# Kernel tuning notes

Measured on AMD Instinct MI355X. Metric: run time of the kernel, lower is better.

The kernel has to match this reference:

```python
import jax, jax.numpy as jnp
import numpy as np

K_DIM = 1024
HEADS = 16
D_K = K_DIM // HEADS


def setup_inputs() -> dict:
    key = jax.random.key(0)
    ks = jax.random.split(key, 6)
    b, t, k = 4, 1024, K_DIM
    scale = 1.0 / np.sqrt(k)
    return {
        "x": jax.random.normal(ks[0], (b, t, k), dtype=jnp.float32),
        "Wq": jax.random.normal(ks[1], (k, k), dtype=jnp.float32) * scale,
        "Wk": jax.random.normal(ks[2], (k, k), dtype=jnp.float32) * scale,
        "Wv": jax.random.normal(ks[3], (k, k), dtype=jnp.float32) * scale,
        "Wo": jax.random.normal(ks[4], (k, k), dtype=jnp.float32) * scale,
        "bo": jax.random.normal(ks[5], (k,), dtype=jnp.float32) * 0.01,
    }


def reference(x, Wq, Wk, Wv, Wo, bo):
    b, t, k = x.shape
    h, d_k = HEADS, D_K
    # Linear(k,k) applies x @ W.T; project then split heads -> [b, h, t, d_k]
    Q = (x @ Wq.T).reshape(b, t, h, d_k).transpose(0, 2, 1, 3)
    Kh = (x @ Wk.T).reshape(b, t, h, d_k).transpose(0, 2, 1, 3)
    V = (x @ Wv.T).reshape(b, t, h, d_k).transpose(0, 2, 1, 3)
    scores = jnp.einsum("bhqd,bhkd->bhqk", Q, Kh) / jnp.sqrt(jnp.float32(d_k))
    attn = jax.nn.softmax(scores, axis=-1)
    out = jnp.einsum("bhqk,bhkd->bhqd", attn, V)
    out = out.transpose(0, 2, 1, 3).reshape(b, t, k)
    return out @ Wo.T + bo
```

## Files before the change

kernel.cpp:

```cpp
#include <hip/hip_runtime.h>
#include <hip/hip_bf16.h>

typedef __attribute__((ext_vector_type(4))) float f32x4;
typedef __attribute__((ext_vector_type(8))) short short8;

#define B_   4
#define T_   1024
#define H_   16
#define DK_  64
#define KDIM 1024

#define QSCALE 0.18033688011112042f

__device__ __forceinline__ unsigned short f2bf(float f){
  union { float f; unsigned int u; } a; a.f = f;
  unsigned int u = a.u;
  return (unsigned short)((u + 0x7FFFu + ((u >> 16) & 1u)) >> 16);
}

__device__ __forceinline__ unsigned int cvtpk_bf16(float lo, float hi){
  unsigned int r;
  asm("v_cvt_pk_bf16_f32 %0, %1, %2" : "=v"(r) : "v"(lo), "v"(hi));
  return r;
}

__device__ __forceinline__ void gload16(const void* g, void* l){
  __builtin_amdgcn_global_load_lds(
      (const __attribute__((address_space(1))) unsigned int*)g,
      (__attribute__((address_space(3))) unsigned int*)l,
      16, 0, 0);
}

__global__ __launch_bounds__(256) void convert5(
    const float* __restrict__ x,  const float* __restrict__ wq,
    const float* __restrict__ wk, const float* __restrict__ wv,
    const float* __restrict__ wo,
    short* __restrict__ xb,  short* __restrict__ wqb,
    short* __restrict__ wkb, short* __restrict__ wvb, short* __restrict__ wob)
{
  int i = blockIdx.x * 256 + threadIdx.x;
  const float* s; short* d; int off;
  if (i < (1 << 20)) { s = x; d = xb; off = i; }
  else {
    int j = i - (1 << 20);
    int w = j >> 18;
    off = j & ((1 << 18) - 1);
    s = (w == 0) ? wq : (w == 1) ? wk : (w == 2) ? wv : wo;
    d = (w == 0) ? wqb : (w == 1) ? wkb : (w == 2) ? wvb : wob;
  }
  float4 v = ((const float4*)s)[off];
  ushort4 o;
  o.x = f2bf(v.x); o.y = f2bf(v.y); o.z = f2bf(v.z); o.w = f2bf(v.w);
  ((ushort4*)d)[off] = o;
}

template<bool SWAP>
__device__ __forceinline__ void gemm3_core(
    const short* __restrict__ A, const short* __restrict__ W,
    int m0, int n0, short* As, short* Bs, f32x4 acc[4][2])
{
  const int tid = threadIdx.x, wv = tid >> 6, lane = tid & 63;
  const int lr = lane & 15, lq = lane >> 4;
  const int wm = wv >> 2, wn = wv & 3;
  const int swz = (lr & 7) << 3;
  const int r = tid >> 3;
  const int c8 = ((tid & 7) * 8) ^ ((r & 7) * 8);

#pragma unroll
  for (int m = 0; m < 4; ++m)
#pragma unroll
    for (int n = 0; n < 2; ++n) acc[m][n] = (f32x4){0.f, 0.f, 0.f, 0.f};

  auto stage = [&](int sb, int kt) {
    const int k0 = kt * 64;
#pragma unroll
    for (int p = 0; p < 2; ++p) {
      const int rp = p * 64 + r;
      gload16(A + (size_t)(m0 + rp) * KDIM + k0 + c8, As + sb * 8192 + p * 4096 + wv * 512);
      gload16(W + (size_t)(n0 + rp) * KDIM + k0 + c8, Bs + sb * 8192 + p * 4096 + wv * 512);
    }
  };

  stage(0, 0);
  stage(1, 1);

  for (int kt = 0; kt < 16; ++kt) {
    if (kt < 15) asm volatile("s_waitcnt vmcnt(4)" ::: "memory");
    else         asm volatile("s_waitcnt vmcnt(0)" ::: "memory");
    __builtin_amdgcn_s_barrier();
    __builtin_amdgcn_sched_barrier(0);
    const int rb = kt % 3;
    const short* Ab = As + rb * 8192;
    const short* Bb = Bs + rb * 8192;
    short8 af[2][4], bfv[2][2];
#pragma unroll
    for (int kk = 0; kk < 2; ++kk) {
#pragma unroll
      for (int m = 0; m < 4; ++m)
        af[kk][m] = *(const short8*)(Ab + (wm * 64 + m * 16 + lr) * 64 + ((kk * 32 + lq * 8) ^ swz));
#pragma unroll
      for (int n = 0; n < 2; ++n)
        bfv[kk][n] = *(const short8*)(Bb + (wn * 32 + n * 16 + lr) * 64 + ((kk * 32 + lq * 8) ^ swz));
    }
    if (kt + 2 < 16) {
      const int sb = (kt + 2) % 3;
      stage(sb, kt + 2);
    }
    __builtin_amdgcn_s_setprio(1);
#pragma unroll
    for (int kk = 0; kk < 2; ++kk)
#pragma unroll
      for (int m = 0; m < 4; ++m)
#pragma unroll
        for (int n = 0; n < 2; ++n) {
          if constexpr (SWAP)
            acc[m][n] = __builtin_amdgcn_mfma_f32_16x16x32_bf16(bfv[kk][n], af[kk][m], acc[m][n], 0, 0, 0);
          else
            acc[m][n] = __builtin_amdgcn_mfma_f32_16x16x32_bf16(af[kk][m], bfv[kk][n], acc[m][n], 0, 0, 0);
        }
    __builtin_amdgcn_s_setprio(0);
  }
}

__global__ __launch_bounds__(512, 1) void gemm3_qkv(
    const short* __restrict__ xb,
    const short* __restrict__ Wqb, const short* __restrict__ Wkb, const short* __restrict__ Wvb,
    short* __restrict__ Qb, short* __restrict__ Kb, short* __restrict__ VTb)
{
  __shared__ __align__(16) short As[3 * 8192];
  __shared__ __align__(16) short Bs[3 * 8192];
  const int bid = blockIdx.x;
  const int wgid = (bid & 7) * 96 + (bid >> 3);
  const int mx = wgid / 24, inner = wgid % 24;
  const int wsel = inner >> 3;
  const int m0 = mx * 128, n0 = (inner & 7) * 128;
  const short* W = (wsel == 0) ? Wqb : (wsel == 1) ? Wkb : Wvb;

  const int tid = threadIdx.x, lane = tid & 63, wv = tid >> 6;
  const int lr = lane & 15, lq = lane >> 4;
  const int wm = wv >> 2, wn = wv & 3;

  if (wsel < 2) {
    f32x4 acc[4][2];
    gemm3_core<true>(xb, W, m0, n0, As, Bs, acc);
    short* O = wsel ? Kb : Qb;
    const float sc = wsel ? 1.0f : QSCALE;
#pragma unroll
    for (int m = 0; m < 4; ++m) {
      const int row = m0 + wm * 64 + m * 16 + lr;
#pragma unroll
      for (int n = 0; n < 2; ++n) {
        const int colb = n0 + wn * 32 + n * 16 + lq * 4;
        ushort4 u;
        u.x = f2bf(acc[m][n][0] * sc); u.y = f2bf(acc[m][n][1] * sc);
        u.z = f2bf(acc[m][n][2] * sc); u.w = f2bf(acc[m][n][3] * sc);
        *(ushort4*)&O[(size_t)row * KDIM + colb] = u;
      }
    }
  } else {
    f32x4 acc[4][2];
    gemm3_core<false>(xb, W, m0, n0, As, Bs, acc);
#pragma unroll
    for (int m = 0; m < 4; ++m)
#pragma unroll
      for (int n = 0; n < 2; ++n) {
        int row = m0 + wm * 64 + m * 16 + lq * 4;
        int col = n0 + wn * 32 + n * 16 + lr;
        int b = row >> 10, t = row & 1023, h = col >> 6, d = col & 63;
        int tp = (t & ~31) + ((t >> 2) & 3) * 8 + ((t >> 4) & 1) * 4 + (t & 3);
        ushort4 v;
        v.x = f2bf(acc[m][n][0]); v.y = f2bf(acc[m][n][1]);
        v.z = f2bf(acc[m][n][2]); v.w = f2bf(acc[m][n][3]);
        *(ushort4*)&VTb[(size_t)((b * 16 + h) * 64 + d) * 1024 + tp] = v;
      }
  }
}

__global__ __launch_bounds__(512, 1) void gemm3_out(
    const short* __restrict__ AOb, const short* __restrict__ Wob,
    const float* __restrict__ bias, float* __restrict__ out)
{
  __shared__ __align__(16) short As[3 * 8192];
  __shared__ __align__(16) short Bs[3 * 8192];
  const int bid = blockIdx.x;
  const int wgid = (bid & 7) * 32 + (bid >> 3);
  const int mx = wgid >> 3, ny = wgid & 7;
  const int m0 = mx * 128, n0 = ny * 128;

  f32x4 acc[4][2];
  gemm3_core<true>(AOb, Wob, m0, n0, As, Bs, acc);

  const int tid = threadIdx.x, lane = tid & 63, wv = tid >> 6;
  const int lr = lane & 15, lq = lane >> 4;
  const int wm = wv >> 2, wn = wv & 3;
#pragma unroll
  for (int n = 0; n < 2; ++n) {
    const int colb = n0 + wn * 32 + n * 16 + lq * 4;
    const float4 bv = *(const float4*)&bias[colb];
#pragma unroll
    for (int m = 0; m < 4; ++m) {
      const int row = m0 + wm * 64 + m * 16 + lr;
      float4 o;
      o.x = acc[m][n][0] + bv.x; o.y = acc[m][n][1] + bv.y;
      o.z = acc[m][n][2] + bv.z; o.w = acc[m][n][3] + bv.w;
      *(float4*)&out[(size_t)row * KDIM + colb] = o;
    }
  }
}

__global__ __launch_bounds__(256) void attn_kern(
    const short* __restrict__ Qb, const short* __restrict__ Kb,
    const short* __restrict__ VTb, short* __restrict__ AOb)
{
  __shared__ __align__(16) short kl[2][64 * 64];
  __shared__ __align__(16) short vl[2][64 * 64];
  const int flat = blockIdx.x;
  const int wg = (flat & 7) * 128 + (flat >> 3);
  const int bh = wg >> 4, b = bh >> 4, h = bh & 15;
  const int q0 = (wg & 15) * 64;
  const int tid = threadIdx.x, wv = tid >> 6, lane = tid & 63;
  const int lr = lane & 15, lq = lane >> 4;

  const short* Qrow = Qb + (size_t)(b * T_ + q0 + wv * 16 + lr) * KDIM + h * DK_;
  short8 qf0 = *(const short8*)(Qrow + lq * 8);
  short8 qf1 = *(const short8*)(Qrow + 32 + lq * 8);

  const short* Kbase = Kb + (size_t)(b * T_) * KDIM + h * DK_;
  const short* Vbase = VTb + (size_t)(bh * DK_) * 1024;

  const int srow = tid >> 3, scol = (tid & 7) * 8;

  auto stage = [&](int buf, int kv0) {
#pragma unroll
    for (int p = 0; p < 2; ++p) {
      const int r = p * 32 + srow;
      gload16(Kbase + (size_t)(kv0 + r) * KDIM + (scol ^ ((r & 7) << 3)),
              &kl[buf][p * 2048 + wv * 512]);
    }
#pragma unroll
    for (int p = 0; p < 2; ++p) {
      const int r = p * 32 + srow;
      gload16(Vbase + (size_t)r * 1024 + kv0 + (scol ^ ((r & 7) << 3)),
              &vl[buf][p * 2048 + wv * 512]);
    }
  };

  f32x4 oacc[4];
#pragma unroll
  for (int i = 0; i < 4; ++i) oacc[i] = (f32x4){0.f, 0.f, 0.f, 0.f};
  float l_r = 0.f;

  int cur = 0;
  stage(0, 0);
  __syncthreads();

  for (int kt = 0; kt < 16; ++kt) {
    if (kt < 15) stage(cur ^ 1, (kt + 1) * 64);

    f32x4 s[4];
#pragma unroll
    for (int nt = 0; nt < 4; ++nt) {
      const int kr = nt * 16 + lr;
      const int swr = (kr & 7) << 3;
      short8 kf0 = *(const short8*)&kl[cur][kr * 64 + ((lq * 8) ^ swr)];
      short8 kf1 = *(const short8*)&kl[cur][kr * 64 + ((32 + lq * 8) ^ swr)];
      f32x4 z = (f32x4){0.f, 0.f, 0.f, 0.f};
      z = __builtin_amdgcn_mfma_f32_16x16x32_bf16(kf0, qf0, z, 0, 0, 0);
      s[nt] = __builtin_amdgcn_mfma_f32_16x16x32_bf16(kf1, qf1, z, 0, 0, 0);
    }

    float rs = 0.f;
#pragma unroll
    for (int nt = 0; nt < 4; ++nt)
#pragma unroll
      for (int j = 0; j < 4; ++j) {
        float e = exp2f(s[nt][j]);
        s[nt][j] = e;
        rs += e;
      }
    l_r += rs;

    union { unsigned int u[4]; short8 v; } pk0, pk1;
    pk0.u[0] = cvtpk_bf16(s[0][0], s[0][1]);
    pk0.u[1] = cvtpk_bf16(s[0][2], s[0][3]);
    pk0.u[2] = cvtpk_bf16(s[1][0], s[1][1]);
    pk0.u[3] = cvtpk_bf16(s[1][2], s[1][3]);
    pk1.u[0] = cvtpk_bf16(s[2][0], s[2][1]);
    pk1.u[1] = cvtpk_bf16(s[2][2], s[2][3]);
    pk1.u[2] = cvtpk_bf16(s[3][0], s[3][1]);
    pk1.u[3] = cvtpk_bf16(s[3][2], s[3][3]);

#pragma unroll
    for (int ntd = 0; ntd < 4; ++ntd) {
      const int vr = ntd * 16 + lr;
      const int swr = (vr & 7) << 3;
      short8 vf0 = *(const short8*)&vl[cur][vr * 64 + ((lq * 8) ^ swr)];
      short8 vf1 = *(const short8*)&vl[cur][vr * 64 + ((32 + lq * 8) ^ swr)];
      oacc[ntd] = __builtin_amdgcn_mfma_f32_16x16x32_bf16(vf0, pk0.v, oacc[ntd], 0, 0, 0);
      oacc[ntd] = __builtin_amdgcn_mfma_f32_16x16x32_bf16(vf1, pk1.v, oacc[ntd], 0, 0, 0);
    }
    __syncthreads();
    cur ^= 1;
  }

  float l = l_r;
  l += __shfl_xor(l, 16);
  l += __shfl_xor(l, 32);
  const float inv = 1.0f / l;

#pragma unroll
  for (int nt = 0; nt < 4; ++nt) {
    ushort4 u;
    u.x = f2bf(oacc[nt][0] * inv);
    u.y = f2bf(oacc[nt][1] * inv);
    u.z = f2bf(oacc[nt][2] * inv);
    u.w = f2bf(oacc[nt][3] * inv);
    *(ushort4*)&AOb[(size_t)(b * T_ + q0 + wv * 16 + lr) * KDIM + h * DK_ + nt * 16 + lq * 4] = u;
  }
}

extern "C" void kernel_launch(void* const* d_in, const int* in_sizes, int n_in,
                              void* d_out, int out_size, void* d_ws, size_t ws_size,
                              hipStream_t stream) {
  const float* x  = (const float*)d_in[0];
  const float* Wq = (const float*)d_in[1];
  const float* Wk = (const float*)d_in[2];
  const float* Wv = (const float*)d_in[3];
  const float* Wo = (const float*)d_in[4];
  const float* bo = (const float*)d_in[5];

  short* ws = (short*)d_ws;
  short* xb  = ws;
  short* Wqb = ws + 4194304;
  short* Wkb = ws + 5242880;
  short* Wvb = ws + 6291456;
  short* Wob = ws + 7340032;
  short* Qb  = ws + 8388608;
  short* Kb  = ws + 12582912;
  short* VTb = ws + 16777216;
  short* AOb = ws + 20971520;

  convert5<<<8192, 256, 0, stream>>>(x, Wq, Wk, Wv, Wo, xb, Wqb, Wkb, Wvb, Wob);
  gemm3_qkv<<<768, 512, 0, stream>>>(xb, Wqb, Wkb, Wvb, Qb, Kb, VTb);
  attn_kern<<<1024, 256, 0, stream>>>(Qb, Kb, VTb, AOb);
  gemm3_out<<<256, 512, 0, stream>>>(AOb, Wob, bo, (float*)d_out);
}
```

Measured before the change: 168.6 us.

## Process two query tiles per warp in attention and fold Q scale into weights

Each attention warp now handles 32 query rows as two 16-row groups instead of 16, so each K/V fragment read from LDS feeds twice as many MFMAs. The grid is halved to 512 blocks of 128 queries, which cuts redundant K/V staging but raises register pressure and lowers the number of blocks. The softmax scale for Q now multiplies Wq during the bf16 conversion rather than the QKV GEMM epilogue. That moves the multiply to a cheaper place and slightly changes rounding.

Result: no change. 168.0 us (-0.4%).

```diff
diff --git a/kernel.cpp b/kernel.cpp
--- a/kernel.cpp
+++ b/kernel.cpp
@@ -40,6 +40,7 @@
 {
   int i = blockIdx.x * 256 + threadIdx.x;
   const float* s; short* d; int off;
+  float sc = 1.0f;
   if (i < (1 << 20)) { s = x; d = xb; off = i; }
   else {
     int j = i - (1 << 20);
@@ -47,10 +48,12 @@
     off = j & ((1 << 18) - 1);
     s = (w == 0) ? wq : (w == 1) ? wk : (w == 2) ? wv : wo;
     d = (w == 0) ? wqb : (w == 1) ? wkb : (w == 2) ? wvb : wob;
+    if (w == 0) sc = QSCALE;
   }
   float4 v = ((const float4*)s)[off];
   ushort4 o;
-  o.x = f2bf(v.x); o.y = f2bf(v.y); o.z = f2bf(v.z); o.w = f2bf(v.w);
+  o.x = f2bf(v.x * sc); o.y = f2bf(v.y * sc);
+  o.z = f2bf(v.z * sc); o.w = f2bf(v.w * sc);
   ((ushort4*)d)[off] = o;
 }
 
@@ -144,7 +147,6 @@
     f32x4 acc[4][2];
     gemm3_core<true>(xb, W, m0, n0, As, Bs, acc);
     short* O = wsel ? Kb : Qb;
-    const float sc = wsel ? 1.0f : QSCALE;
 #pragma unroll
     for (int m = 0; m < 4; ++m) {
       const int row = m0 + wm * 64 + m * 16 + lr;
@@ -152,8 +154,8 @@
       for (int n = 0; n < 2; ++n) {
         const int colb = n0 + wn * 32 + n * 16 + lq * 4;
         ushort4 u;
-        u.x = f2bf(acc[m][n][0] * sc); u.y = f2bf(acc[m][n][1] * sc);
-        u.z = f2bf(acc[m][n][2] * sc); u.w = f2bf(acc[m][n][3] * sc);
+        u.x = f2bf(acc[m][n][0]); u.y = f2bf(acc[m][n][1]);
+        u.z = f2bf(acc[m][n][2]); u.w = f2bf(acc[m][n][3]);
         *(ushort4*)&O[(size_t)row * KDIM + colb] = u;
       }
     }
@@ -215,15 +217,19 @@
   __shared__ __align__(16) short kl[2][64 * 64];
   __shared__ __align__(16) short vl[2][64 * 64];
   const int flat = blockIdx.x;
-  const int wg = (flat & 7) * 128 + (flat >> 3);
-  const int bh = wg >> 4, b = bh >> 4, h = bh & 15;
-  const int q0 = (wg & 15) * 64;
+  const int wg = (flat & 7) * 64 + (flat >> 3);
+  const int bh = wg >> 3, b = bh >> 4, h = bh & 15;
+  const int q0 = (wg & 7) * 128;
   const int tid = threadIdx.x, wv = tid >> 6, lane = tid & 63;
   const int lr = lane & 15, lq = lane >> 4;
 
-  const short* Qrow = Qb + (size_t)(b * T_ + q0 + wv * 16 + lr) * KDIM + h * DK_;
-  short8 qf0 = *(const short8*)(Qrow + lq * 8);
-  short8 qf1 = *(const short8*)(Qrow + 32 + lq * 8);
+  short8 qf[2][2];
+#pragma unroll
+  for (int g = 0; g < 2; ++g) {
+    const short* Qrow = Qb + (size_t)(b * T_ + q0 + wv * 32 + g * 16 + lr) * KDIM + h * DK_;
+    qf[g][0] = *(const short8*)(Qrow + lq * 8);
+    qf[g][1] = *(const short8*)(Qrow + 32 + lq * 8);
+  }
 
   const short* Kbase = Kb + (size_t)(b * T_) * KDIM + h * DK_;
   const short* Vbase = VTb + (size_t)(bh * DK_) * 1024;
@@ -245,10 +251,12 @@
     }
   };
 
-  f32x4 oacc[4];
-#pragma unroll
-  for (int i = 0; i < 4; ++i) oacc[i] = (f32x4){0.f, 0.f, 0.f, 0.f};
-  float l_r = 0.f;
+  f32x4 oacc[2][4];
+#pragma unroll
+  for (int g = 0; g < 2; ++g)
+#pragma unroll
+    for (int i = 0; i < 4; ++i) oacc[g][i] = (f32x4){0.f, 0.f, 0.f, 0.f};
+  float l_r[2] = {0.f, 0.f};
 
   int cur = 0;
   stage(0, 0);
@@ -257,38 +265,43 @@
   for (int kt = 0; kt < 16; ++kt) {
     if (kt < 15) stage(cur ^ 1, (kt + 1) * 64);
 
-    f32x4 s[4];
+    f32x4 s[2][4];
 #pragma unroll
     for (int nt = 0; nt < 4; ++nt) {
       const int kr = nt * 16 + lr;
       const int swr = (kr & 7) << 3;
       short8 kf0 = *(const short8*)&kl[cur][kr * 64 + ((lq * 8) ^ swr)];
       short8 kf1 = *(const short8*)&kl[cur][kr * 64 + ((32 + lq * 8) ^ swr)];
-      f32x4 z = (f32x4){0.f, 0.f, 0.f, 0.f};
-      z = __builtin_amdgcn_mfma_f32_16x16x32_bf16(kf0, qf0, z, 0, 0, 0);
-      s[nt] = __builtin_amdgcn_mfma_f32_16x16x32_bf16(kf1, qf1, z, 0, 0, 0);
-    }
-
-    float rs = 0.f;
-#pragma unroll
-    for (int nt = 0; nt < 4; ++nt)
-#pragma unroll
-      for (int j = 0; j < 4; ++j) {
-        float e = exp2f(s[nt][j]);
-        s[nt][j] = e;
-        rs += e;
+#pragma unroll
+      for (int g = 0; g < 2; ++g) {
+        f32x4 z = (f32x4){0.f, 0.f, 0.f, 0.f};
+        z = __builtin_amdgcn_mfma_f32_16x16x32_bf16(kf0, qf[g][0], z, 0, 0, 0);
+        s[g][nt] = __builtin_amdgcn_mfma_f32_16x16x32_bf16(kf1, qf[g][1], z, 0, 0, 0);
       }
-    l_r += rs;
-
-    union { unsigned int u[4]; short8 v; } pk0, pk1;
-    pk0.u[0] = cvtpk_bf16(s[0][0], s[0][1]);
-    pk0.u[1] = cvtpk_bf16(s[0][2], s[0][3]);
-    pk0.u[2] = cvtpk_bf16(s[1][0], s[1][1]);
-    pk0.u[3] = cvtpk_bf16(s[1][2], s[1][3]);
-    pk1.u[0] = cvtpk_bf16(s[2][0], s[2][1]);
-    pk1.u[1] = cvtpk_bf16(s[2][2], s[2][3]);
-    pk1.u[2] = cvtpk_bf16(s[3][0], s[3][1]);
-    pk1.u[3] = cvtpk_bf16(s[3][2], s[3][3]);
+    }
+
+    union { unsigned int u[4]; short8 v; } pk[2][2];
+#pragma unroll
+    for (int g = 0; g < 2; ++g) {
+      float rs = 0.f;
+#pragma unroll
+      for (int nt = 0; nt < 4; ++nt)
+#pragma unroll
+        for (int j = 0; j < 4; ++j) {
+          float e = exp2f(s[g][nt][j]);
+          s[g][nt][j] = e;
+          rs += e;
+        }
+      l_r[g] += rs;
+      pk[g][0].u[0] = cvtpk_bf16(s[g][0][0], s[g][0][1]);
+      pk[g][0].u[1] = cvtpk_bf16(s[g][0][2], s[g][0][3]);
+      pk[g][0].u[2] = cvtpk_bf16(s[g][1][0], s[g][1][1]);
+      pk[g][0].u[3] = cvtpk_bf16(s[g][1][2], s[g][1][3]);
+      pk[g][1].u[0] = cvtpk_bf16(s[g][2][0], s[g][2][1]);
+      pk[g][1].u[1] = cvtpk_bf16(s[g][2][2], s[g][2][3]);
+      pk[g][1].u[2] = cvtpk_bf16(s[g][3][0], s[g][3][1]);
+      pk[g][1].u[3] = cvtpk_bf16(s[g][3][2], s[g][3][3]);
+    }
 
 #pragma unroll
     for (int ntd = 0; ntd < 4; ++ntd) {
@@ -296,26 +309,32 @@
       const int swr = (vr & 7) << 3;
       short8 vf0 = *(const short8*)&vl[cur][vr * 64 + ((lq * 8) ^ swr)];
       short8 vf1 = *(const short8*)&vl[cur][vr * 64 + ((32 + lq * 8) ^ swr)];
-      oacc[ntd] = __builtin_amdgcn_mfma_f32_16x16x32_bf16(vf0, pk0.v, oacc[ntd], 0, 0, 0);
-      oacc[ntd] = __builtin_amdgcn_mfma_f32_16x16x32_bf16(vf1, pk1.v, oacc[ntd], 0, 0, 0);
+#pragma unroll
+      for (int g = 0; g < 2; ++g) {
+        oacc[g][ntd] = __builtin_amdgcn_mfma_f32_16x16x32_bf16(vf0, pk[g][0].v, oacc[g][ntd], 0, 0, 0);
+        oacc[g][ntd] = __builtin_amdgcn_mfma_f32_16x16x32_bf16(vf1, pk[g][1].v, oacc[g][ntd], 0, 0, 0);
+      }
     }
     __syncthreads();
     cur ^= 1;
   }
 
-  float l = l_r;
-  l += __shfl_xor(l, 16);
-  l += __shfl_xor(l, 32);
-  const float inv = 1.0f / l;
-
-#pragma unroll
-  for (int nt = 0; nt < 4; ++nt) {
-    ushort4 u;
-    u.x = f2bf(oacc[nt][0] * inv);
-    u.y = f2bf(oacc[nt][1] * inv);
-    u.z = f2bf(oacc[nt][2] * inv);
-    u.w = f2bf(oacc[nt][3] * inv);
-    *(ushort4*)&AOb[(size_t)(b * T_ + q0 + wv * 16 + lr) * KDIM + h * DK_ + nt * 16 + lq * 4] = u;
+#pragma unroll
+  for (int g = 0; g < 2; ++g) {
+    float l = l_r[g];
+    l += __shfl_xor(l, 16);
+    l += __shfl_xor(l, 32);
+    const float inv = 1.0f / l;
+    const size_t rowb = (size_t)(b * T_ + q0 + wv * 32 + g * 16 + lr) * KDIM + h * DK_;
+#pragma unroll
+    for (int nt = 0; nt < 4; ++nt) {
+      ushort4 u;
+      u.x = f2bf(oacc[g][nt][0] * inv);
+      u.y = f2bf(oacc[g][nt][1] * inv);
+      u.z = f2bf(oacc[g][nt][2] * inv);
+      u.w = f2bf(oacc[g][nt][3] * inv);
+      *(ushort4*)&AOb[rowb + nt * 16 + lq * 4] = u;
+    }
   }
 }
 
@@ -342,6 +361,6 @@
 
   convert5<<<8192, 256, 0, stream>>>(x, Wq, Wk, Wv, Wo, xb, Wqb, Wkb, Wvb, Wob);
   gemm3_qkv<<<768, 512, 0, stream>>>(xb, Wqb, Wkb, Wvb, Qb, Kb, VTb);
-  attn_kern<<<1024, 256, 0, stream>>>(Qb, Kb, VTb, AOb);
+  attn_kern<<<512, 256, 0, stream>>>(Qb, Kb, VTb, AOb);
   gemm3_out<<<256, 512, 0, stream>>>(AOb, Wob, bo, (float*)d_out);
 }
```
